# Optimization experiments

Hardware: AMD Instinct MI355X
Metric: run time of the kernel (lower is better)

Reference implementation:

```python
import jax, jax.numpy as jnp
import numpy as np

N = 768
SINGLE_DIM = 384
PAIR_DIM = 128
D = 16      # proj_dim per head
H = 12      # n_heads
P = 4       # n_query_points
PV = 8      # n_point_values


def _random_rotations(key, n):
    a = jax.random.normal(key, (n, 3, 3), dtype=jnp.float32)
    q, r = jnp.linalg.qr(a)
    d = jnp.sign(jnp.diagonal(r, axis1=-2, axis2=-1))
    q = q * d[:, None, :]
    det = jnp.linalg.det(q)
    return q * jnp.where(det < 0, -1.0, 1.0)[:, None, None]


def setup_inputs() -> dict:
    key = jax.random.key(0)
    ks = jax.random.split(key, 12)
    s = 0.02
    return {
        "single_rep": jax.random.normal(ks[0], (N, SINGLE_DIM), dtype=jnp.float32),
        "pair_rep": jax.random.normal(ks[1], (N, N, PAIR_DIM), dtype=jnp.float32),
        "rotations": _random_rotations(ks[2], N),
        "translations": jax.random.normal(ks[3], (N, 3), dtype=jnp.float32),
        "Wqkv": s * jax.random.normal(ks[4], (SINGLE_DIM, 3 * H * D), dtype=jnp.float32),
        "Wb": s * jax.random.normal(ks[5], (PAIR_DIM, H), dtype=jnp.float32),
        "Wqk_pts": s * jax.random.normal(ks[6], (SINGLE_DIM, 2 * H * P * 3), dtype=jnp.float32),
        "Wv_pts": s * jax.random.normal(ks[7], (SINGLE_DIM, H * PV * 3), dtype=jnp.float32),
        "gamma": 0.1 * jax.random.normal(ks[8], (H,), dtype=jnp.float32),
        "Wout": s * jax.random.normal(ks[9], (H * (PAIR_DIM + D + PV * 3 + PV), SINGLE_DIM), dtype=jnp.float32),
        "bout": jnp.zeros((SINGLE_DIM,), dtype=jnp.float32),
    }


def _apply_frames(rot, trans, pts):
    # pts: [N, P, H, 3] -> R @ pt + t per residue (dim 0)
    return jnp.einsum('nba,npha->nphb', rot, pts) + trans[:, None, None, :]


def _apply_frames_inv(rot, trans, pts):
    # R^T (pt - t)
    return jnp.einsum('nab,npha->nphb', rot, pts - trans[:, None, None, :])


def reference(single_rep, pair_rep, rotations, translations,
              Wqkv, Wb, Wqk_pts, Wv_pts, gamma, Wout, bout):
    n = single_rep.shape[0]
    sqrt_inv_dim = 1.0 / np.sqrt(D).astype(np.float32)
    w_C = np.sqrt(2.0 / (9.0 * P)).astype(np.float32)
    w_L = np.sqrt(1.0 / 3.0).astype(np.float32)

    qkv = single_rep @ Wqkv                       # [N, 3*H*D]
    q, k, v = jnp.split(qkv, 3, axis=-1)
    q = q.reshape(n, D, H)
    k = k.reshape(n, D, H)
    v = v.reshape(n, D, H)

    b = pair_rep @ Wb                             # [N, N, H]

    qk_pts = single_rep @ Wqk_pts
    q_pts, k_pts = jnp.split(qk_pts, 2, axis=-1)
    q_pts = jnp.moveaxis(q_pts.reshape(n, P, 3, H), -1, -2)   # [N, P, H, 3]
    k_pts = jnp.moveaxis(k_pts.reshape(n, P, 3, H), -1, -2)
    v_pts = jnp.moveaxis((single_rep @ Wv_pts).reshape(n, PV, 3, H), -1, -2)  # [N, PV, H, 3]

    qg = _apply_frames(rotations, translations, q_pts)  # [N, P, H, 3]
    kg = _apply_frames(rotations, translations, k_pts)

    # sum_{p,t} ||qg_i - kg_j||^2 via expansion (avoids [N,N,P,H,3])
    q_sq = jnp.sum(qg * qg, axis=(1, 3))                # [N, H]
    k_sq = jnp.sum(kg * kg, axis=(1, 3))                # [N, H]
    cross = jnp.einsum('ipht,jpht->ijh', qg, kg)        # [N, N, H]
    dist_logits = q_sq[:, None, :] + k_sq[None, :, :] - 2.0 * cross

    dp_logits = sqrt_inv_dim * jnp.einsum('idh,jdh->ijh', q, k) + b
    scale = gamma * (w_C / 2.0)                          # [H]
    a = jax.nn.softmax(w_L * (dp_logits - scale * dist_logits), axis=1)  # [N, N, H]

    out_pair = jnp.einsum('ijh,ijz->izh', a, pair_rep)   # [N, pair_dim, H]
    out_value = jnp.einsum('ijh,jdh->idh', a, v)          # [N, D, H]

    vg = _apply_frames(rotations, translations, v_pts)    # [N, PV, H, 3]
    op = jnp.einsum('ijh,jpht->ipht', a, vg)              # [N, PV, H, 3]
    out_points = _apply_frames_inv(rotations, translations, op)
    out_points_norm = jnp.linalg.norm(out_points, axis=-1)  # [N, PV, H]

    out = jnp.concatenate([
        out_pair.reshape(n, -1),
        out_value.reshape(n, -1),
        out_points.reshape(n, -1),
        out_points_norm.reshape(n, -1),
    ], axis=1)
    return out @ Wout + bout
```

## Files before the change

### kernel.cpp

```cpp
#include <hip/hip_runtime.h>
#include <math.h>

#define NN 768
#define SD 384
#define HH 12

#define W_L 0.57735026918962576f
#define W_C 0.23570226039551584f

typedef __attribute__((ext_vector_type(8))) short short8;
typedef __attribute__((ext_vector_type(4))) float floatx4;
typedef unsigned short ushort_t;
typedef unsigned int uint_t;

__device__ __forceinline__ float wave_max(float v){ for(int o=32;o;o>>=1) v=fmaxf(v,__shfl_xor(v,o)); return v; }
__device__ __forceinline__ float wave_sum(float v){ for(int o=32;o;o>>=1) v+=__shfl_xor(v,o); return v; }

static __device__ __forceinline__ ushort_t f2bf(float f) {
  union { float f; uint_t u; } v; v.f = f;
  uint_t r = (v.u + 0x7FFFu + ((v.u >> 16) & 1u)) >> 16;
  return (ushort_t)r;
}
static __device__ __forceinline__ float bf2f(ushort_t u) {
  union { uint_t u; float f; } v; v.u = ((uint_t)u) << 16; return v.f;
}

__global__ __launch_bounds__(256) void k1a_gemm(
    const float* __restrict__ single, const float* __restrict__ Wqkv,
    const float* __restrict__ Wqk, const float* __restrict__ Wvp,
    float* __restrict__ raw)
{
  __shared__ float Al[64][17];
  __shared__ float Bl[16][68];
  const int tid = threadIdx.x;
  const int bm = blockIdx.x / 18, bn = blockIdx.x % 18;
  const int tr = tid >> 4, tc = tid & 15;

  const int bcol = bn*64 + (tid & 15)*4;
  const float* Wsrc; int wstride;
  if (bcol < 576)      { Wsrc = Wqkv + bcol;        wstride = 576; }
  else if (bcol < 864) { Wsrc = Wqk  + (bcol-576);  wstride = 288; }
  else                 { Wsrc = Wvp  + (bcol-864);  wstride = 288; }
  const int brow = tid >> 4;
  const int ar = tid >> 2, ac = (tid & 3)*4;

  float4 acc0 = {0,0,0,0}, acc1 = {0,0,0,0}, acc2 = {0,0,0,0}, acc3 = {0,0,0,0};

  for (int kc = 0; kc < 24; ++kc) {
    __syncthreads();
    *(float4*)&Al[ar][ac] = *(const float4*)(single + (size_t)(bm*64+ar)*SD + kc*16 + ac);
    *(float4*)&Bl[brow][(tid&15)*4] = *(const float4*)(Wsrc + (size_t)(kc*16+brow)*wstride);
    __syncthreads();
    #pragma unroll
    for (int kk = 0; kk < 16; ++kk) {
      float a0 = Al[tr*4+0][kk], a1 = Al[tr*4+1][kk], a2 = Al[tr*4+2][kk], a3 = Al[tr*4+3][kk];
      float4 bv = *(float4*)&Bl[kk][tc*4];
      acc0.x += a0*bv.x; acc0.y += a0*bv.y; acc0.z += a0*bv.z; acc0.w += a0*bv.w;
      acc1.x += a1*bv.x; acc1.y += a1*bv.y; acc1.z += a1*bv.z; acc1.w += a1*bv.w;
      acc2.x += a2*bv.x; acc2.y += a2*bv.y; acc2.z += a2*bv.z; acc2.w += a2*bv.w;
      acc3.x += a3*bv.x; acc3.y += a3*bv.y; acc3.z += a3*bv.z; acc3.w += a3*bv.w;
    }
  }
  float* o = raw + (size_t)(bm*64 + tr*4)*1152 + bn*64 + tc*4;
  *(float4*)(o)            = acc0;
  *(float4*)(o + 1152)     = acc1;
  *(float4*)(o + 2*1152)   = acc2;
  *(float4*)(o + 3*1152)   = acc3;
}

__global__ __launch_bounds__(256) void k1b_pack(
    const float* __restrict__ raw_g, const float* __restrict__ rot,
    const float* __restrict__ trans, const float* __restrict__ gamma,
    float* __restrict__ Qt, ushort_t* __restrict__ Ktb, ushort_t* __restrict__ vvb)
{
  __shared__ float raw[4][1152];
  __shared__ float gbuf[4][16][HH][3];
  const int tid = threadIdx.x;
  const int i0 = blockIdx.x * 4;

  for (int s = tid; s < 4*288; s += 256) {
    int r = s / 288, q = s % 288;
    *(float4*)(&raw[r][q*4]) = *(const float4*)(raw_g + (size_t)(i0+r)*1152 + q*4);
  }
  __syncthreads();

  for (int s = tid; s < 4*576; s += 256) {
    int r = s / 576, cc = s % 576;
    int d = (cc % 192) / HH, h = cc % HH;
    int i = i0 + r;
    float val = raw[r][cc];
    if (cc < 192)       Qt[(size_t)i*384 + h*32 + d] = 0.25f*W_L*val;
    else if (cc < 384)  Ktb[(size_t)i*384 + h*32 + d] = f2bf(val);
    else                vvb[(size_t)i*480 + h*40 + d] = f2bf(val);
  }
  for (int s = tid; s < 768; s += 256) {
    int r = s / 192, rem = s % 192;
    int slot = rem / HH, h = rem % HH;
    int i = i0 + r;
    int base;
    if (slot < 4) base = 576 + slot*36;
    else if (slot < 8) base = 720 + (slot-4)*36;
    else base = 864 + (slot-8)*36;
    float x0 = raw[r][base + 0*12 + h];
    float x1 = raw[r][base + 1*12 + h];
    float x2 = raw[r][base + 2*12 + h];
    const float* R = rot + (size_t)i*9;
    const float* T = trans + (size_t)i*3;
    float g0 = R[0]*x0 + R[1]*x1 + R[2]*x2 + T[0];
    float g1 = R[3]*x0 + R[4]*x1 + R[5]*x2 + T[1];
    float g2 = R[6]*x0 + R[7]*x1 + R[8]*x2 + T[2];
    gbuf[r][slot][h][0]=g0; gbuf[r][slot][h][1]=g1; gbuf[r][slot][h][2]=g2;
    if (slot < 4) {
      float sc2 = 2.0f*W_L*(gamma[h]*W_C*0.5f);
      float* q = Qt + (size_t)i*384 + h*32 + 16 + slot*3;
      q[0]=sc2*g0; q[1]=sc2*g1; q[2]=sc2*g2;
    } else if (slot < 8) {
      ushort_t* k = Ktb + (size_t)i*384 + h*32 + 16 + (slot-4)*3;
      k[0]=f2bf(g0); k[1]=f2bf(g1); k[2]=f2bf(g2);
    } else {
      ushort_t* vp = vvb + (size_t)i*480 + h*40 + 16 + (slot-8)*3;
      vp[0]=f2bf(g0); vp[1]=f2bf(g1); vp[2]=f2bf(g2);
    }
  }
  __syncthreads();
  for (int s = tid; s < 96; s += 256) {
    int r = s / 24, rem = s % 24;
    int h = rem / 2, qk = rem % 2;
    int i = i0 + r;
    float sum = 0;
    int b0 = qk ? 4 : 0;
    for (int p = 0; p < 4; ++p)
      for (int t = 0; t < 3; ++t) { float g = gbuf[r][b0+p][h][t]; sum += g*g; }
    float sc = gamma[h]*W_C*0.5f;
    if (qk == 0) {
      float* q = Qt + (size_t)i*384 + h*32;
      q[28] = -W_L*sc; q[29] = -W_L*sc*sum; q[30] = 0.f; q[31] = 0.f;
    } else {
      ushort_t* k = Ktb + (size_t)i*384 + h*32;
      k[28] = f2bf(sum); k[29] = f2bf(1.f); k[30] = 0; k[31] = 0;
    }
  }
}

__global__ __launch_bounds__(256) void k2a_logits(
    const float* __restrict__ pair, const float* __restrict__ Wb,
    const float* __restrict__ Qt, const ushort_t* __restrict__ Ktb,
    float* __restrict__ L)
{
  __shared__ ushort_t Tj[64*136];
  __shared__ ushort_t WbT[16*136];
  __shared__ float Qrow[384];
  const int tid = threadIdx.x;
  const int i = blockIdx.x / 12;
  const int j0 = (blockIdx.x % 12) * 64;
  const int lane = tid & 63;
  const int w = tid >> 6;
  const int co = lane & 15, gg = lane >> 4;

  for (int s = tid; s < 1536; s += 256) {
    int z = s / 12, h = s % 12;
    WbT[h*136 + z] = f2bf(W_L * Wb[s]);
  }
  for (int s = tid; s < 544; s += 256) WbT[1632 + s] = 0;
  for (int s = tid; s < 384; s += 256) Qrow[s] = Qt[(size_t)i*384 + s];

  const float* src = pair + ((size_t)i*NN + j0)*128;
  #pragma unroll
  for (int k = 0; k < 8; ++k) {
    int f = tid + k*256;
    int row = f >> 5, zq = f & 31;
    float4 v = *(const float4*)(src + (size_t)row*128 + zq*4);
    uint_t u0 = ((uint_t)f2bf(v.y) << 16) | f2bf(v.x);
    uint_t u1 = ((uint_t)f2bf(v.w) << 16) | f2bf(v.z);
    uint_t* d = (uint_t*)&Tj[row*136 + zq*4];
    d[0] = u0; d[1] = u1;
  }
  __syncthreads();

  short8 z8, myQ, wb[4];
  #pragma unroll
  for (int s = 0; s < 8; ++s) z8[s] = 0;
  #pragma unroll
  for (int s = 0; s < 8; ++s)
    myQ[s] = (co < 12) ? (short)f2bf(Qrow[co*32 + gg*8 + s]) : (short)0;
  #pragma unroll
  for (int kt = 0; kt < 4; ++kt)
    wb[kt] = *(const short8*)&WbT[co*136 + kt*32 + gg*8];

  const int jb = w*16;
  floatx4 D; D[0]=0.f; D[1]=0.f; D[2]=0.f; D[3]=0.f;
  #pragma unroll
  for (int kt = 0; kt < 4; ++kt) {
    short8 a = *(const short8*)&Tj[(jb+co)*136 + kt*32 + gg*8];
    D = __builtin_amdgcn_mfma_f32_16x16x32_bf16(a, wb[kt], D, 0, 0, 0);
  }
  const ushort_t* kr = Ktb + (size_t)(j0 + jb + co)*384;
  #pragma unroll
  for (int kt = 0; kt < 12; ++kt) {
    short8 a = *(const short8*)(kr + kt*32 + gg*8);
    short8 b = (co == kt) ? myQ : z8;
    D = __builtin_amdgcn_mfma_f32_16x16x32_bf16(a, b, D, 0, 0, 0);
  }
  if (co < 12) {
    float4 st = {D[0], D[1], D[2], D[3]};
    *(float4*)(L + ((size_t)i*12 + co)*768 + j0 + jb + gg*4) = st;
  }
}

__global__ __launch_bounds__(256) void k2b_pairout(
    const float* __restrict__ pair, float* __restrict__ L,
    float* __restrict__ C2)
{
  __shared__ ushort_t PTb[24*16*32];
  __shared__ ushort_t Tz[32*134];
  const int tid = threadIdx.x;
  const int i = (NN - 1) - blockIdx.x;
  const int lane = tid & 63;
  const int w = tid >> 6;
  const int co = lane & 15, gg = lane >> 4;

  float* Lr = L + (size_t)i*12*768;
  ushort_t* abr = (ushort_t*)Lr;
  const int ln = lane;
  {
    const int wv = w;
    #pragma unroll 1
    for (int m = 0; m < 3; ++m) {
      int h = wv + 4*m;
      const float* row = Lr + (size_t)h*768;
      float mx = -1e30f;
      for (int jj = ln; jj < 768; jj += 64) mx = fmaxf(mx, row[jj]);
      mx = wave_max(mx);
      float sm = 0.f;
      float ev[12];
      #pragma unroll
      for (int k = 0; k < 12; ++k) {
        float e = __expf(row[ln + 64*k] - mx);
        ev[k] = e; sm += e;
      }
      sm = wave_sum(sm);
      float inv = 1.0f / sm;
      #pragma unroll
      for (int k = 0; k < 12; ++k) {
        int jj = ln + 64*k;
        ushort_t a = f2bf(ev[k]*inv);
        PTb[(jj >> 5)*512 + h*32 + (jj & 31)] = a;
      }
      #pragma unroll
      for (int k = 0; k < 12; ++k) {
        int jj = ln + 64*k;
        abr[h*768 + jj] = f2bf(ev[k]*inv);
      }
    }
  }
  __syncthreads();

  floatx4 accZ[2];
  #pragma unroll
  for (int u = 0; u < 2; ++u) { accZ[u][0]=0.f; accZ[u][1]=0.f; accZ[u][2]=0.f; accZ[u][3]=0.f; }

  const int srow = tid >> 5, szq = tid & 31;
  const float* psrc = pair + (size_t)i*NN*128;

  float4 pr[4];
  #pragma unroll
  for (int k = 0; k < 4; ++k) {
    int f = tid + k*256;
    int row = f >> 5, zq = f & 31;
    pr[k] = *(const float4*)(psrc + (size_t)row*128 + zq*4);
  }

  #pragma unroll 1
  for (int t = 0; t < 24; ++t) {
    #pragma unroll
    for (int k = 0; k < 4; ++k) {
      int f = tid + k*256;
      int row = f >> 5, zq = f & 31;
      uint_t u0 = ((uint_t)f2bf(pr[k].y) << 16) | f2bf(pr[k].x);
      uint_t u1 = ((uint_t)f2bf(pr[k].w) << 16) | f2bf(pr[k].z);
      uint_t* d = (uint_t*)Tz;
      d[row*67 + zq*2]     = u0;
      d[row*67 + zq*2 + 1] = u1;
    }
    __syncthreads();
    if (t < 23) {
      const float* sn = psrc + (size_t)(t+1)*32*128;
      #pragma unroll
      for (int k = 0; k < 4; ++k) {
        int f = tid + k*256;
        int row = f >> 5, zq = f & 31;
        pr[k] = *(const float4*)(sn + (size_t)row*128 + zq*4);
      }
    }
    short8 aP = *(const short8*)&PTb[t*512 + co*32 + gg*8];
    #pragma unroll
    for (int u = 0; u < 2; ++u) {
      const int n = w*2 + u;
      short8 bT;
      #pragma unroll
      for (int e = 0; e < 8; ++e)
        bT[e] = (short)Tz[(gg*8 + e)*134 + n*16 + co];
      accZ[u] = __builtin_amdgcn_mfma_f32_16x16x32_bf16(aP, bT, accZ[u], 0, 0, 0);
    }
    __syncthreads();
  }

  float* o = C2 + (size_t)i*2112;
  #pragma unroll
  for (int u = 0; u < 2; ++u) {
    const int n = w*2 + u;
    #pragma unroll
    for (int r = 0; r < 4; ++r) {
      int h = gg*4 + r;
      if (h < 12) o[(n*16 + co)*12 + h] = accZ[u][r];
    }
  }
}

__global__ __launch_bounds__(256) void k4_value_points(
    const float* __restrict__ L, const ushort_t* __restrict__ vvb,
    const float* __restrict__ rot, const float* __restrict__ trans,
    float* __restrict__ C2)
{
  __shared__ ushort_t abl[12*768];
  __shared__ ushort_t vt[32*488];
  __shared__ float oacc[480];
  const int tid = threadIdx.x;
  const int i = blockIdx.x;
  const ushort_t* abr = (const ushort_t*)(L + (size_t)i*12*768);

  for (int s = tid; s < 4608; s += 256)
    ((uint_t*)abl)[s] = ((const uint_t*)abr)[s];

  const int h = tid / 20, c2 = tid % 20;
  float acc0 = 0.f, acc1 = 0.f;

  #pragma unroll 1
  for (int t = 0; t < 24; ++t) {
    __syncthreads();
    const ushort_t* src = vvb + (size_t)t*32*480;
    for (int s = tid; s < 1920; s += 256) {
      int row = s / 60, cq = s % 60;
      *(float4*)&vt[row*488 + cq*8] = *(const float4*)(src + (size_t)row*480 + cq*8);
    }
    __syncthreads();
    if (tid < 240) {
      const int j0 = t*32;
      #pragma unroll 4
      for (int jj = 0; jj < 32; ++jj) {
        float a = bf2f(abl[h*768 + j0 + jj]);
        uint_t pv = *(const uint_t*)&vt[jj*488 + h*40 + c2*2];
        acc0 += a * bf2f((ushort_t)(pv & 0xffffu));
        acc1 += a * bf2f((ushort_t)(pv >> 16));
      }
    }
  }
  __syncthreads();
  if (tid < 240) {
    oacc[h*40 + c2*2]     = acc0;
    oacc[h*40 + c2*2 + 1] = acc1;
  }
  __syncthreads();

  if (tid < 96) {
    const int pp = tid / 12, hh = tid % 12;
    const float* R = rot + (size_t)i*9;
    const float* T = trans + (size_t)i*3;
    float x0 = oacc[hh*40+16+pp*3+0] - T[0];
    float x1 = oacc[hh*40+16+pp*3+1] - T[1];
    float x2 = oacc[hh*40+16+pp*3+2] - T[2];
    float y0 = R[0]*x0 + R[3]*x1 + R[6]*x2;
    float y1 = R[1]*x0 + R[4]*x1 + R[7]*x2;
    float y2 = R[2]*x0 + R[5]*x1 + R[8]*x2;
    float* o = C2 + (size_t)i*2112;
    o[1728 + pp*36 + hh*3 + 0] = y0;
    o[1728 + pp*36 + hh*3 + 1] = y1;
    o[1728 + pp*36 + hh*3 + 2] = y2;
    o[2016 + pp*12 + hh] = sqrtf(y0*y0 + y1*y1 + y2*y2);
  } else if (tid >= 96 && tid < 288) {
    const int c = tid - 96;
    if (c < 192) {
      int d = c / 12, hh = c % 12;
      C2[(size_t)i*2112 + 1536 + d*12 + hh] = oacc[hh*40 + d];
    }
  }
}

__global__ __launch_bounds__(256) void k5_out(
    const float* __restrict__ C2, const float* __restrict__ Wout,
    const float* __restrict__ bout, float* __restrict__ out)
{
  __shared__ float Al[32*68];
  __shared__ float Bl[64*36];
  const int tid = threadIdx.x;
  const int bm = blockIdx.x / 12, bn = blockIdx.x % 12;
  const int tr = tid / 16, tc = tid % 16;
  float acc00=0, acc01=0, acc10=0, acc11=0;
  for (int kc = 0; kc < 33; ++kc) {
    __syncthreads();
    for (int s = tid; s < 512; s += 256) {
      int row = s / 16, kq = s % 16;
      *(float4*)(&Al[row*68 + kq*4]) =
        *(const float4*)(C2 + (size_t)(bm*32+row)*2112 + kc*64 + kq*4);
    }
    for (int s = tid; s < 512; s += 256) {
      int kk = s / 8, cq = s % 8;
      *(float4*)(&Bl[kk*36 + cq*4]) =
        *(const float4*)(Wout + (size_t)(kc*64+kk)*384 + bn*32 + cq*4);
    }
    __syncthreads();
    for (int kk = 0; kk < 64; ++kk) {
      float a0 = Al[(tr*2)*68 + kk], a1 = Al[(tr*2+1)*68 + kk];
      float b0 = Bl[kk*36 + tc*2], b1 = Bl[kk*36 + tc*2 + 1];
      acc00 += a0*b0; acc01 += a0*b1;
      acc10 += a1*b0; acc11 += a1*b1;
    }
  }
  int r0 = bm*32 + tr*2, c0 = bn*32 + tc*2;
  out[(size_t)r0*384 + c0]       = acc00 + bout[c0];
  out[(size_t)r0*384 + c0+1]     = acc01 + bout[c0+1];
  out[(size_t)(r0+1)*384 + c0]   = acc10 + bout[c0];
  out[(size_t)(r0+1)*384 + c0+1] = acc11 + bout[c0+1];
}

extern "C" void kernel_launch(void* const* d_in, const int* in_sizes, int n_in,
                              void* d_out, int out_size, void* d_ws, size_t ws_size,
                              hipStream_t stream)
{
  const float* single = (const float*)d_in[0];
  const float* pair   = (const float*)d_in[1];
  const float* rot    = (const float*)d_in[2];
  const float* trans  = (const float*)d_in[3];
  const float* Wqkv   = (const float*)d_in[4];
  const float* Wb     = (const float*)d_in[5];
  const float* Wqk    = (const float*)d_in[6];
  const float* Wvp    = (const float*)d_in[7];
  const float* gamma  = (const float*)d_in[8];
  const float* Wout   = (const float*)d_in[9];
  const float* bout   = (const float*)d_in[10];

  float* ws   = (float*)d_ws;
  float* raw  = ws;
  float* Qt   = raw + (size_t)768*1152;
  float* C2   = Qt  + (size_t)768*384;
  float* L    = C2  + (size_t)768*2112;
  ushort_t* Ktb = (ushort_t*)(L + (size_t)768*12*768);
  ushort_t* vvb = Ktb + (size_t)768*384;
  float* out  = (float*)d_out;

  k1a_gemm<<<dim3(216), dim3(256), 0, stream>>>(single, Wqkv, Wqk, Wvp, raw);
  k1b_pack<<<dim3(192), dim3(256), 0, stream>>>(raw, rot, trans, gamma, Qt, Ktb, vvb);
  k2a_logits<<<dim3(9216), dim3(256), 0, stream>>>(pair, Wb, Qt, Ktb, L);
  k2b_pairout<<<dim3(768), dim3(256), 0, stream>>>(pair, L, C2);
  k4_value_points<<<dim3(768), dim3(256), 0, stream>>>(L, vvb, rot, trans, C2);
  k5_out<<<dim3(288), dim3(256), 0, stream>>>(C2, Wout, bout, out);
}
```

Before: 390.3 us.

## Fuse softmax, pair-output and value/point aggregation into one MFMA kernel

Merges the softmax+pair-output kernel and the value/points kernel into one 512-thread kernel per residue. The value and point aggregation moves from scalar FMAs over an LDS copy of the attention row to bf16 MFMA, reading a new transposed V layout (channel-major) written by the pack kernel. The pair tile staging is double-buffered with a swizzled LDS layout so one barrier per step suffices. This drops the bf16 attention write-back to global and one kernel launch, at the cost of higher register and LDS pressure and strided global writes in the pack kernel.

```diff
diff --git a/kernel.cpp b/kernel.cpp
--- a/kernel.cpp
+++ b/kernel.cpp
@@ -9,6 +9,7 @@
 #define W_C 0.23570226039551584f
 
 typedef __attribute__((ext_vector_type(8))) short short8;
+typedef __attribute__((ext_vector_type(4))) short short4_t;
 typedef __attribute__((ext_vector_type(4))) float floatx4;
 typedef unsigned short ushort_t;
 typedef unsigned int uint_t;
@@ -20,9 +21,6 @@
   union { float f; uint_t u; } v; v.f = f;
   uint_t r = (v.u + 0x7FFFu + ((v.u >> 16) & 1u)) >> 16;
   return (ushort_t)r;
-}
-static __device__ __forceinline__ float bf2f(ushort_t u) {
-  union { uint_t u; float f; } v; v.u = ((uint_t)u) << 16; return v.f;
 }
 
 __global__ __launch_bounds__(256) void k1a_gemm(
@@ -71,7 +69,7 @@
 __global__ __launch_bounds__(256) void k1b_pack(
     const float* __restrict__ raw_g, const float* __restrict__ rot,
     const float* __restrict__ trans, const float* __restrict__ gamma,
-    float* __restrict__ Qt, ushort_t* __restrict__ Ktb, ushort_t* __restrict__ vvb)
+    float* __restrict__ Qt, ushort_t* __restrict__ Ktb, ushort_t* __restrict__ vvT)
 {
   __shared__ float raw[4][1152];
   __shared__ float gbuf[4][16][HH][3];
@@ -91,7 +89,7 @@
     float val = raw[r][cc];
     if (cc < 192)       Qt[(size_t)i*384 + h*32 + d] = 0.25f*W_L*val;
     else if (cc < 384)  Ktb[(size_t)i*384 + h*32 + d] = f2bf(val);
-    else                vvb[(size_t)i*480 + h*40 + d] = f2bf(val);
+    else                vvT[(size_t)(h*40 + d)*768 + i] = f2bf(val);
   }
   for (int s = tid; s < 768; s += 256) {
     int r = s / 192, rem = s % 192;
@@ -118,8 +116,8 @@
       ushort_t* k = Ktb + (size_t)i*384 + h*32 + 16 + (slot-4)*3;
       k[0]=f2bf(g0); k[1]=f2bf(g1); k[2]=f2bf(g2);
     } else {
-      ushort_t* vp = vvb + (size_t)i*480 + h*40 + 16 + (slot-8)*3;
-      vp[0]=f2bf(g0); vp[1]=f2bf(g1); vp[2]=f2bf(g2);
+      ushort_t* vp = vvT + (size_t)(h*40 + 16 + (slot-8)*3)*768 + i;
+      vp[0]=f2bf(g0); vp[768]=f2bf(g1); vp[2*768]=f2bf(g2);
     }
   }
   __syncthreads();
@@ -207,158 +205,138 @@
   }
 }
 
-__global__ __launch_bounds__(256) void k2b_pairout(
-    const float* __restrict__ pair, float* __restrict__ L,
-    float* __restrict__ C2)
-{
-  __shared__ ushort_t PTb[24*16*32];
-  __shared__ ushort_t Tz[32*134];
+__global__ __launch_bounds__(512) void k3_fused(
+    const float* __restrict__ pair, const float* __restrict__ L,
+    const ushort_t* __restrict__ vvT, const float* __restrict__ rot,
+    const float* __restrict__ trans, float* __restrict__ C2)
+{
+  __shared__ ushort_t PTb[24*512];
+  __shared__ ushort_t Tz[2][2][128*20];
+  __shared__ float oacc[480];
   const int tid = threadIdx.x;
   const int i = (NN - 1) - blockIdx.x;
-  const int lane = tid & 63;
-  const int w = tid >> 6;
+  const int w = tid >> 6, lane = tid & 63;
   const int co = lane & 15, gg = lane >> 4;
 
-  float* Lr = L + (size_t)i*12*768;
-  ushort_t* abr = (ushort_t*)Lr;
-  const int ln = lane;
+  const float* psrc = pair + (size_t)i*NN*128;
+
+  float4 pr0, pr1;
   {
-    const int wv = w;
-    #pragma unroll 1
-    for (int m = 0; m < 3; ++m) {
-      int h = wv + 4*m;
-      const float* row = Lr + (size_t)h*768;
-      float mx = -1e30f;
-      for (int jj = ln; jj < 768; jj += 64) mx = fmaxf(mx, row[jj]);
-      mx = wave_max(mx);
-      float sm = 0.f;
-      float ev[12];
-      #pragma unroll
-      for (int k = 0; k < 12; ++k) {
-        float e = __expf(row[ln + 64*k] - mx);
-        ev[k] = e; sm += e;
-      }
-      sm = wave_sum(sm);
-      float inv = 1.0f / sm;
-      #pragma unroll
-      for (int k = 0; k < 12; ++k) {
-        int jj = ln + 64*k;
-        ushort_t a = f2bf(ev[k]*inv);
-        PTb[(jj >> 5)*512 + h*32 + (jj & 31)] = a;
-      }
-      #pragma unroll
-      for (int k = 0; k < 12; ++k) {
-        int jj = ln + 64*k;
-        abr[h*768 + jj] = f2bf(ev[k]*inv);
-      }
-    }
-  }
-  __syncthreads();
-
-  floatx4 accZ[2];
-  #pragma unroll
-  for (int u = 0; u < 2; ++u) { accZ[u][0]=0.f; accZ[u][1]=0.f; accZ[u][2]=0.f; accZ[u][3]=0.f; }
-
-  const int srow = tid >> 5, szq = tid & 31;
-  const float* psrc = pair + (size_t)i*NN*128;
-
-  float4 pr[4];
-  #pragma unroll
-  for (int k = 0; k < 4; ++k) {
-    int f = tid + k*256;
-    int row = f >> 5, zq = f & 31;
-    pr[k] = *(const float4*)(psrc + (size_t)row*128 + zq*4);
-  }
+    int f0 = tid,      j0 = f0 >> 5, zq0 = f0 & 31;
+    int f1 = tid + 512, j1 = f1 >> 5, zq1 = f1 & 31;
+    pr0 = *(const float4*)(psrc + (size_t)j0*128 + zq0*4);
+    pr1 = *(const float4*)(psrc + (size_t)j1*128 + zq1*4);
+  }
+
+  const float* Lr = L + (size_t)i*12*768;
+  #pragma unroll
+  for (int m = 0; m < 2; ++m) {
+    if (m == 1 && w >= 4) break;
+    const int h = (m == 0) ? w : 8 + w;
+    const float* row = Lr + (size_t)h*768;
+    float mx = -1e30f;
+    #pragma unroll
+    for (int k = 0; k < 12; ++k) mx = fmaxf(mx, row[lane + 64*k]);
+    mx = wave_max(mx);
+    float ev[12]; float sm = 0.f;
+    #pragma unroll
+    for (int k = 0; k < 12; ++k) { ev[k] = __expf(row[lane + 64*k] - mx); sm += ev[k]; }
+    sm = wave_sum(sm);
+    const float inv = 1.0f / sm;
+    #pragma unroll
+    for (int k = 0; k < 12; ++k) {
+      int jj = lane + 64*k;
+      PTb[(jj >> 5)*512 + h*32 + (jj & 31)] = f2bf(ev[k]*inv);
+    }
+  }
+  for (int s = tid; s < 3072; s += 512) {
+    int t = s >> 7, rest = s & 127;
+    PTb[t*512 + 384 + rest] = 0;
+  }
+
+  floatx4 accZ; accZ[0]=0.f; accZ[1]=0.f; accZ[2]=0.f; accZ[3]=0.f;
+  floatx4 accV[4];
+  #pragma unroll
+  for (int u = 0; u < 4; ++u) { accV[u][0]=0.f; accV[u][1]=0.f; accV[u][2]=0.f; accV[u][3]=0.f; }
+
+  const int sw = (w & 3) << 2;
+  const int jb = (gg & 1) * 8;
+  const ushort_t* vb0 = vvT + (size_t)((w*4+0)*16 + co)*768 + gg*8;
+  const ushort_t* vb1 = vvT + (size_t)((w*4+1)*16 + co)*768 + gg*8;
+  const ushort_t* vb2 = vvT + (size_t)((w*4+2)*16 + co)*768 + gg*8;
+  const ushort_t* vb3 = vvT + (size_t)((w*4+3)*16 + co)*768 + gg*8;
 
   #pragma unroll 1
   for (int t = 0; t < 24; ++t) {
-    #pragma unroll
-    for (int k = 0; k < 4; ++k) {
-      int f = tid + k*256;
-      int row = f >> 5, zq = f & 31;
-      uint_t u0 = ((uint_t)f2bf(pr[k].y) << 16) | f2bf(pr[k].x);
-      uint_t u1 = ((uint_t)f2bf(pr[k].w) << 16) | f2bf(pr[k].z);
-      uint_t* d = (uint_t*)Tz;
-      d[row*67 + zq*2]     = u0;
-      d[row*67 + zq*2 + 1] = u1;
-    }
-    __syncthreads();
+    const int buf = t & 1;
+    {
+      int f0 = tid,      j0 = f0 >> 5, zq0 = f0 & 31;
+      int f1 = tid + 512, j1 = f1 >> 5, zq1 = f1 & 31;
+      const float* p0 = (const float*)&pr0;
+      const float* p1 = (const float*)&pr1;
+      ushort_t* tz0 = &Tz[buf][j0 >> 4][0];
+      ushort_t* tz1 = &Tz[buf][j1 >> 4][0];
+      const int jl0 = j0 & 15, jl1 = j1 & 15;
+      #pragma unroll
+      for (int e = 0; e < 4; ++e) {
+        int z0 = zq0*4 + e;
+        tz0[z0*20 + (jl0 ^ (((z0 >> 4) & 3) << 2))] = f2bf(p0[e]);
+        int z1 = zq1*4 + e;
+        tz1[z1*20 + (jl1 ^ (((z1 >> 4) & 3) << 2))] = f2bf(p1[e]);
+      }
+    }
     if (t < 23) {
       const float* sn = psrc + (size_t)(t+1)*32*128;
-      #pragma unroll
-      for (int k = 0; k < 4; ++k) {
-        int f = tid + k*256;
-        int row = f >> 5, zq = f & 31;
-        pr[k] = *(const float4*)(sn + (size_t)row*128 + zq*4);
-      }
-    }
-    short8 aP = *(const short8*)&PTb[t*512 + co*32 + gg*8];
-    #pragma unroll
-    for (int u = 0; u < 2; ++u) {
-      const int n = w*2 + u;
+      int f0 = tid,      j0 = f0 >> 5, zq0 = f0 & 31;
+      int f1 = tid + 512, j1 = f1 >> 5, zq1 = f1 & 31;
+      pr0 = *(const float4*)(sn + (size_t)j0*128 + zq0*4);
+      pr1 = *(const float4*)(sn + (size_t)j1*128 + zq1*4);
+    }
+    __syncthreads();
+
+    const short8 aP = *(const short8*)&PTb[t*512 + co*32 + gg*8];
+    {
+      const ushort_t* tz = &Tz[buf][gg >> 1][0];
+      const int zrow = (w*16 + co)*20;
+      short4_t lo = *(const short4_t*)&tz[zrow + (jb ^ sw)];
+      short4_t hi = *(const short4_t*)&tz[zrow + ((jb + 4) ^ sw)];
       short8 bT;
       #pragma unroll
-      for (int e = 0; e < 8; ++e)
-        bT[e] = (short)Tz[(gg*8 + e)*134 + n*16 + co];
-      accZ[u] = __builtin_amdgcn_mfma_f32_16x16x32_bf16(aP, bT, accZ[u], 0, 0, 0);
-    }
-    __syncthreads();
+      for (int e = 0; e < 4; ++e) { bT[e] = lo[e]; bT[e+4] = hi[e]; }
+      accZ = __builtin_amdgcn_mfma_f32_16x16x32_bf16(aP, bT, accZ, 0, 0, 0);
+    }
+    {
+      const int toff = t*32;
+      short8 bV;
+      bV = *(const short8*)(vb0 + toff);
+      accV[0] = __builtin_amdgcn_mfma_f32_16x16x32_bf16(aP, bV, accV[0], 0, 0, 0);
+      bV = *(const short8*)(vb1 + toff);
+      accV[1] = __builtin_amdgcn_mfma_f32_16x16x32_bf16(aP, bV, accV[1], 0, 0, 0);
+      if (w*4 + 2 < 30) {
+        bV = *(const short8*)(vb2 + toff);
+        accV[2] = __builtin_amdgcn_mfma_f32_16x16x32_bf16(aP, bV, accV[2], 0, 0, 0);
+        bV = *(const short8*)(vb3 + toff);
+        accV[3] = __builtin_amdgcn_mfma_f32_16x16x32_bf16(aP, bV, accV[3], 0, 0, 0);
+      }
+    }
   }
 
   float* o = C2 + (size_t)i*2112;
   #pragma unroll
-  for (int u = 0; u < 2; ++u) {
-    const int n = w*2 + u;
-    #pragma unroll
-    for (int r = 0; r < 4; ++r) {
-      int h = gg*4 + r;
-      if (h < 12) o[(n*16 + co)*12 + h] = accZ[u][r];
-    }
-  }
-}
-
-__global__ __launch_bounds__(256) void k4_value_points(
-    const float* __restrict__ L, const ushort_t* __restrict__ vvb,
-    const float* __restrict__ rot, const float* __restrict__ trans,
-    float* __restrict__ C2)
-{
-  __shared__ ushort_t abl[12*768];
-  __shared__ ushort_t vt[32*488];
-  __shared__ float oacc[480];
-  const int tid = threadIdx.x;
-  const int i = blockIdx.x;
-  const ushort_t* abr = (const ushort_t*)(L + (size_t)i*12*768);
-
-  for (int s = tid; s < 4608; s += 256)
-    ((uint_t*)abl)[s] = ((const uint_t*)abr)[s];
-
-  const int h = tid / 20, c2 = tid % 20;
-  float acc0 = 0.f, acc1 = 0.f;
-
-  #pragma unroll 1
-  for (int t = 0; t < 24; ++t) {
-    __syncthreads();
-    const ushort_t* src = vvb + (size_t)t*32*480;
-    for (int s = tid; s < 1920; s += 256) {
-      int row = s / 60, cq = s % 60;
-      *(float4*)&vt[row*488 + cq*8] = *(const float4*)(src + (size_t)row*480 + cq*8);
-    }
-    __syncthreads();
-    if (tid < 240) {
-      const int j0 = t*32;
-      #pragma unroll 4
-      for (int jj = 0; jj < 32; ++jj) {
-        float a = bf2f(abl[h*768 + j0 + jj]);
-        uint_t pv = *(const uint_t*)&vt[jj*488 + h*40 + c2*2];
-        acc0 += a * bf2f((ushort_t)(pv & 0xffffu));
-        acc1 += a * bf2f((ushort_t)(pv >> 16));
-      }
-    }
-  }
-  __syncthreads();
-  if (tid < 240) {
-    oacc[h*40 + c2*2]     = acc0;
-    oacc[h*40 + c2*2 + 1] = acc1;
+  for (int r = 0; r < 4; ++r) {
+    int h = gg*4 + r;
+    if (h < 12) o[(w*16 + co)*12 + h] = accZ[r];
+  }
+  #pragma unroll
+  for (int u = 0; u < 4; ++u) {
+    int cb = w*4 + u;
+    if (cb < 30) {
+      int c = cb*16 + co;
+      int hc = c / 40;
+      #pragma unroll
+      for (int r = 0; r < 4; ++r)
+        if (gg*4 + r == hc) oacc[c] = accV[u][r];
+    }
   }
   __syncthreads();
 
@@ -372,17 +350,14 @@
     float y0 = R[0]*x0 + R[3]*x1 + R[6]*x2;
     float y1 = R[1]*x0 + R[4]*x1 + R[7]*x2;
     float y2 = R[2]*x0 + R[5]*x1 + R[8]*x2;
-    float* o = C2 + (size_t)i*2112;
     o[1728 + pp*36 + hh*3 + 0] = y0;
     o[1728 + pp*36 + hh*3 + 1] = y1;
     o[1728 + pp*36 + hh*3 + 2] = y2;
     o[2016 + pp*12 + hh] = sqrtf(y0*y0 + y1*y1 + y2*y2);
-  } else if (tid >= 96 && tid < 288) {
+  } else if (tid < 288) {
     const int c = tid - 96;
-    if (c < 192) {
-      int d = c / 12, hh = c % 12;
-      C2[(size_t)i*2112 + 1536 + d*12 + hh] = oacc[hh*40 + d];
-    }
+    int d = c / 12, hh = c % 12;
+    o[1536 + d*12 + hh] = oacc[hh*40 + d];
   }
 }
 
@@ -445,13 +420,12 @@
   float* C2   = Qt  + (size_t)768*384;
   float* L    = C2  + (size_t)768*2112;
   ushort_t* Ktb = (ushort_t*)(L + (size_t)768*12*768);
-  ushort_t* vvb = Ktb + (size_t)768*384;
+  ushort_t* vvT = Ktb + (size_t)768*384;
   float* out  = (float*)d_out;
 
   k1a_gemm<<<dim3(216), dim3(256), 0, stream>>>(single, Wqkv, Wqk, Wvp, raw);
-  k1b_pack<<<dim3(192), dim3(256), 0, stream>>>(raw, rot, trans, gamma, Qt, Ktb, vvb);
+  k1b_pack<<<dim3(192), dim3(256), 0, stream>>>(raw, rot, trans, gamma, Qt, Ktb, vvT);
   k2a_logits<<<dim3(9216), dim3(256), 0, stream>>>(pair, Wb, Qt, Ktb, L);
-  k2b_pairout<<<dim3(768), dim3(256), 0, stream>>>(pair, L, C2);
-  k4_value_points<<<dim3(768), dim3(256), 0, stream>>>(L, vvb, rot, trans, C2);
+  k3_fused<<<dim3(768), dim3(512), 0, stream>>>(pair, L, vvT, rot, trans, C2);
   k5_out<<<dim3(288), dim3(256), 0, stream>>>(C2, Wout, bout, out);
 }
```

Measured after the change: 320.0 us. -18.0%, faster.
